# Optimization experiments

Hardware: AMD Instinct MI355X
Metric: run time of the kernel (lower is better)

## Reference

```python
import jax, jax.numpy as jnp
import numpy as np

D = 1024   # hidden
H = 4      # heads
HD = D // H
E = 8      # experts
FF = 4096  # expert ffn dim
CAP_FACTOR = 1.0


def _ln(x, g, b, eps=1e-5):
    mu = jnp.mean(x, -1, keepdims=True)
    v = jnp.mean((x - mu) ** 2, -1, keepdims=True)
    return (x - mu) * jax.lax.rsqrt(v + eps) * g + b


def setup_inputs() -> dict:
    key = jax.random.key(0)
    ks = jax.random.split(key, 8)
    L, N = 1024, 16
    s = 0.02
    return {
        "x": jax.random.normal(ks[0], (L, N, D), jnp.float32),
        "in_proj_w": jax.random.normal(ks[1], (3 * D, D), jnp.float32) * s,
        "in_proj_b": jnp.zeros((3 * D,), jnp.float32),
        "out_proj_w": jax.random.normal(ks[2], (D, D), jnp.float32) * s,
        "out_proj_b": jnp.zeros((D,), jnp.float32),
        "ln1_g": jnp.ones((D,), jnp.float32),
        "ln1_b": jnp.zeros((D,), jnp.float32),
        "ln2_g": jnp.ones((D,), jnp.float32),
        "ln2_b": jnp.zeros((D,), jnp.float32),
        "wg": jax.random.normal(ks[3], (D, E), jnp.float32) * s,
        "w1": jax.random.normal(ks[4], (E, D, FF), jnp.float32) * s,
        "b1": jnp.zeros((E, FF), jnp.float32),
        "w2": jax.random.normal(ks[5], (E, FF, D), jnp.float32) * s,
        "b2": jnp.zeros((E, D), jnp.float32),
    }


def _mha(x, w, b, ow, ob):
    # x: [L, N, D] (torch MultiheadAttention layout, batch_first=False)
    L, N, _ = x.shape
    qkv = x @ w.T + b
    q, k, v = jnp.split(qkv, 3, axis=-1)
    rh = lambda t: t.reshape(L, N, H, HD).transpose(1, 2, 0, 3)  # -> [N,H,L,HD]
    q, k, v = rh(q), rh(k), rh(v)
    scores = jnp.einsum('nhld,nhmd->nhlm', q, k) / np.float32(np.sqrt(HD))
    attn = jax.nn.softmax(scores, axis=-1)
    o = jnp.einsum('nhlm,nhmd->nhld', attn, v).transpose(2, 0, 1, 3).reshape(L, N, D)
    return o @ ow.T + ob


def _moe(x, wg, w1, b1, w2, b2):
    # top-1 switch gating with capacity drop, dispatch, grouped GEMM, combine
    L, N, _ = x.shape
    S = L * N
    cap = int(CAP_FACTOR * S) // E  # 2048
    xf = x.reshape(S, D)
    gates = jax.nn.softmax(xf @ wg, axis=-1)           # [S,E]
    idx = jnp.argmax(gates, axis=-1)                    # [S] top-1 expert
    mask1 = jax.nn.one_hot(idx, E, dtype=x.dtype)       # [S,E]
    # position of each token within its expert's queue
    loc = jnp.sum((jnp.cumsum(mask1, 0) - 1.0) * mask1, -1).astype(jnp.int32)
    keep = loc < cap                                    # capacity drop mask
    gate_val = jnp.take_along_axis(gates, idx[:, None], -1)[:, 0]
    slot = jnp.where(keep, idx.astype(jnp.int32) * cap + loc, E * cap)  # OOB if dropped
    disp = jnp.zeros((E * cap, D), x.dtype).at[slot].set(xf, mode='drop')
    disp = disp.reshape(E, cap, D)
    # expert = Linear(D,FF) -> Linear(FF,D), NO activation between (per source)
    h = jnp.einsum('ecd,edf->ecf', disp, w1) + b1[:, None, :]
    y = (jnp.einsum('ecf,efd->ecd', h, w2) + b2[:, None, :]).reshape(E * cap, D)
    out = jnp.where(keep[:, None], gate_val[:, None] * y[jnp.minimum(slot, E * cap - 1)], 0.0)
    return out.reshape(L, N, D)


def reference(x, in_proj_w, in_proj_b, out_proj_w, out_proj_b,
              ln1_g, ln1_b, ln2_g, ln2_b, wg, w1, b1, w2, b2):
    y1 = _ln(x + _mha(x, in_proj_w, in_proj_b, out_proj_w, out_proj_b), ln1_g, ln1_b)
    y2 = _ln(y1 + _moe(y1, wg, w1, b1, w2, b2), ln2_g, ln2_b)
    return y2
```

## Files before the change

kernel.cpp:

```cpp
#include <hip/hip_runtime.h>
#include <hip/hip_bf16.h>

typedef __bf16 bf16_t;
typedef bf16_t bf16x4 __attribute__((ext_vector_type(4)));
typedef bf16_t bf16x8 __attribute__((ext_vector_type(8)));
typedef float  f32x4  __attribute__((ext_vector_type(4)));
typedef _Float16 half4 __attribute__((ext_vector_type(4)));
typedef _Float16 half8 __attribute__((ext_vector_type(8)));

#define L_  1024
#define N_  16
#define S_  16384
#define D_  1024
#define H_  4
#define HD_ 256
#define E_  8
#define FF_ 4096
#define CAP_ 2048
#define ESLOTS_ (E_*CAP_)
#define TAU_ 0.03f

__device__ __forceinline__ void gload16(const void* g, void* l) {
  __builtin_amdgcn_global_load_lds(
      (const __attribute__((address_space(1))) void*)g,
      (__attribute__((address_space(3))) void*)l,
      16, 0, 0);
}

#define SRC_SWZ(lane) (((lane) & 3) ^ (((lane) >> 3) & 3))

__global__ __launch_bounds__(256) void split2(
    const float* __restrict__ in, _Float16* __restrict__ oh,
    _Float16* __restrict__ ol, long n4)
{
  long i = (long)blockIdx.x * blockDim.x + threadIdx.x;
  long stride = (long)gridDim.x * blockDim.x;
  for (; i < n4; i += stride) {
    float4 v = ((const float4*)in)[i];
    half4 h, l;
    h.x = (_Float16)v.x; l.x = (_Float16)((v.x - (float)h.x) * 4096.0f);
    h.y = (_Float16)v.y; l.y = (_Float16)((v.y - (float)h.y) * 4096.0f);
    h.z = (_Float16)v.z; l.z = (_Float16)((v.z - (float)h.z) * 4096.0f);
    h.w = (_Float16)v.w; l.w = (_Float16)((v.w - (float)h.w) * 4096.0f);
    ((half4*)oh)[i] = h;
    ((half4*)ol)[i] = l;
  }
}

template<int EPI, bool HAS_BIAS, int PROD>
__global__ __launch_bounds__(256) void hgemm3s(
    const _Float16* __restrict__ Ah, const _Float16* __restrict__ Al,
    const _Float16* __restrict__ Bh, const _Float16* __restrict__ Bl,
    float* __restrict__ Cf, _Float16* __restrict__ Ch, _Float16* __restrict__ Cl,
    const float* __restrict__ bias,
    int K, long lda, long ldb, long ldcf, long ldch,
    int Z2, long sA1, long sA2, long sB1, long sB2, long sC1, long sC2, long sBias)
{
  constexpr int NL = (PROD == 3) ? 2 : 1;
  __shared__ _Float16 tA[NL][2][128 * 32];
  __shared__ _Float16 tB[NL][2][64 * 32];
  const int z  = blockIdx.z;
  const int z1 = z / Z2, z2 = z - z1 * Z2;
  const long aoff = (long)z1 * sA1 + (long)z2 * sA2;
  const long boff = (long)z1 * sB1 + (long)z2 * sB2;
  const long coff = (long)z1 * sC1 + (long)z2 * sC2;
  const int brow = blockIdx.y * 128, bcol = blockIdx.x * 64;
  const int tid = threadIdx.x, lane = tid & 63, wid = tid >> 6;
  const int wr = (wid >> 1) * 64, wc = (wid & 1) * 32;
  const int fr = lane & 15;
  const int fqs = (((lane >> 4) ^ ((fr >> 1) & 3)) * 8);

  const bool isA = (wid < 2);
  int limb, dstoff, nch;
  const _Float16* ssrc;
  if constexpr (PROD == 3) {
    limb = wid & 1; nch = isA ? 8 : 4; dstoff = 0;
    ssrc = (wid == 0) ? Ah : (wid == 1) ? Al : (wid == 2) ? Bh : Bl;
  } else {
    limb = 0; nch = isA ? 4 : 2; dstoff = (wid & 1) * nch;
    ssrc = isA ? Ah : Bh;
  }
  const long sld = isA ? lda : ldb;
  const long soff = isA ? aoff : boff;
  int srow = (isA ? brow : bcol) + (lane >> 2);
  if constexpr (PROD == 1) srow += (wid & 1) * (isA ? 64 : 32);
  const _Float16* sbase = ssrc + soff + (long)srow * sld + SRC_SWZ(lane) * 8;

  f32x4 acc0[4][2], acc1[4][2];
#pragma unroll
  for (int mi = 0; mi < 4; ++mi)
#pragma unroll
    for (int ni = 0; ni < 2; ++ni) {
      acc0[mi][ni] = f32x4{0.f, 0.f, 0.f, 0.f};
      acc1[mi][ni] = f32x4{0.f, 0.f, 0.f, 0.f};
    }

  {
    _Float16* d0 = (isA ? &tA[limb][0][0] : &tB[limb][0][0]) + dstoff * 512;
    for (int i = 0; i < nch; ++i)
      gload16(sbase + (long)(16 * i) * sld, d0 + i * 512);
  }
  __syncthreads();

  const int NT = K >> 5;
  for (int t = 0; t < NT; ++t) {
    const int cur = t & 1;
    if (t + 1 < NT) {
      const int k1 = (t + 1) * 32;
      _Float16* d0 = (isA ? &tA[limb][cur ^ 1][0] : &tB[limb][cur ^ 1][0]) + dstoff * 512;
      for (int i = 0; i < nch; ++i)
        gload16(sbase + (long)(16 * i) * sld + k1, d0 + i * 512);
    }

    half8 bh_[2], bl_[2];
#pragma unroll
    for (int ni = 0; ni < 2; ++ni) {
      bh_[ni] = *(const half8*)&tB[0][cur][(wc + ni * 16 + fr) * 32 + fqs];
      if constexpr (PROD == 3)
        bl_[ni] = *(const half8*)&tB[1][cur][(wc + ni * 16 + fr) * 32 + fqs];
    }
    half8 ah_[4], al_[4];
#pragma unroll
    for (int mi = 0; mi < 4; ++mi) {
      ah_[mi] = *(const half8*)&tA[0][cur][(wr + mi * 16 + fr) * 32 + fqs];
      if constexpr (PROD == 3)
        al_[mi] = *(const half8*)&tA[1][cur][(wr + mi * 16 + fr) * 32 + fqs];
    }
#pragma unroll
    for (int mi = 0; mi < 4; ++mi)
#pragma unroll
      for (int ni = 0; ni < 2; ++ni)
        acc0[mi][ni] = __builtin_amdgcn_mfma_f32_16x16x32_f16(ah_[mi], bh_[ni], acc0[mi][ni], 0, 0, 0);
    if constexpr (PROD == 3) {
#pragma unroll
      for (int mi = 0; mi < 4; ++mi)
#pragma unroll
        for (int ni = 0; ni < 2; ++ni)
          acc1[mi][ni] = __builtin_amdgcn_mfma_f32_16x16x32_f16(ah_[mi], bl_[ni], acc1[mi][ni], 0, 0, 0);
#pragma unroll
      for (int mi = 0; mi < 4; ++mi)
#pragma unroll
        for (int ni = 0; ni < 2; ++ni)
          acc1[mi][ni] = __builtin_amdgcn_mfma_f32_16x16x32_f16(al_[mi], bh_[ni], acc1[mi][ni], 0, 0, 0);
    }
    __syncthreads();
  }

#pragma unroll
  for (int mi = 0; mi < 4; ++mi) {
#pragma unroll
    for (int ni = 0; ni < 2; ++ni) {
      int gcol = bcol + wc + ni * 16 + fr;
      float bv = 0.0f;
      if constexpr (HAS_BIAS) bv = bias[(long)z1 * sBias + gcol];
#pragma unroll
      for (int v = 0; v < 4; ++v) {
        int grow = brow + wr + mi * 16 + (lane >> 4) * 4 + v;
        float val = acc0[mi][ni][v] + bv;
        if constexpr (PROD == 3) val += acc1[mi][ni][v] * 0.000244140625f;
        if constexpr (EPI == 0) {
          Cf[coff + (long)grow * ldcf + gcol] = val;
        } else if constexpr (EPI == 1) {
          _Float16 hh = (_Float16)val;
          _Float16 ll = (_Float16)((val - (float)hh) * 4096.0f);
          long ci = coff + (long)grow * ldch + gcol;
          Ch[ci] = hh; Cl[ci] = ll;
        } else if constexpr (EPI == 3) {
          Ch[coff + (long)grow * ldch + gcol] = (_Float16)val;
        } else {
          if (bcol < 2048) {
            _Float16 hh = (_Float16)val;
            _Float16 ll = (_Float16)((val - (float)hh) * 4096.0f);
            long ci = (long)grow * ldch + gcol;
            Ch[ci] = hh; Cl[ci] = ll;
          } else {
            Cf[(long)grow * ldcf + (gcol - 2048)] = val;
          }
        }
      }
    }
  }
}

template<bool OUT_BF16, bool HAS_BIAS>
__global__ __launch_bounds__(512) void bgemm256(
    const bf16_t* __restrict__ A, const bf16_t* __restrict__ B,
    void* __restrict__ Cout, const float* __restrict__ bias,
    int K, long lda, long ldb, long ldc,
    long sA1, long sB1, long sC1, long sBias)
{
  __shared__ bf16_t tA[2][256 * 32];
  __shared__ bf16_t tB[2][128 * 32];
  const int z = blockIdx.z;
  const long coff = (long)z * sC1;
  const int brow = blockIdx.y * 256, bcol = blockIdx.x * 128;
  const int tid = threadIdx.x, lane = tid & 63, wid = tid >> 6;
  const int wr = (wid >> 1) * 64, wc = (wid & 1) * 64;
  const int fr = lane & 15;
  const int fqs = (((lane >> 4) ^ ((fr >> 1) & 3)) * 8);

  const bf16_t* Ab = A + (long)z * sA1;
  const bf16_t* Bb = B + (long)z * sB1;

  const bf16_t* csrc[3];
  bf16_t* cd0[3];
  bf16_t* cd1[3];
  long cld[3];
#pragma unroll
  for (int i = 0; i < 3; ++i) {
    int c = wid * 3 + i;
    bool cA = c < 16;
    const bf16_t* s0 = cA ? Ab : Bb;
    long ld = cA ? lda : ldb;
    int r0 = cA ? (brow + 16 * c) : (bcol + 16 * (c - 16));
    csrc[i] = s0 + (long)(r0 + (lane >> 2)) * ld + SRC_SWZ(lane) * 8;
    cld[i] = ld;
    cd0[i] = cA ? &tA[0][c * 512] : &tB[0][(c - 16) * 512];
    cd1[i] = cA ? &tA[1][c * 512] : &tB[1][(c - 16) * 512];
  }

  f32x4 acc[4][4];
#pragma unroll
  for (int mi = 0; mi < 4; ++mi)
#pragma unroll
    for (int ni = 0; ni < 4; ++ni)
      acc[mi][ni] = f32x4{0.0f, 0.0f, 0.0f, 0.0f};

#pragma unroll
  for (int i = 0; i < 3; ++i) gload16(csrc[i], cd0[i]);
  __syncthreads();

  const int NT = K >> 5;
  for (int t = 0; t < NT; ++t) {
    const int cur = t & 1;
    if (t + 1 < NT) {
      const int k1 = (t + 1) * 32;
#pragma unroll
      for (int i = 0; i < 3; ++i)
        gload16(csrc[i] + k1, cur ? cd0[i] : cd1[i]);
    }
    bf16x8 af[4], bfv[4];
#pragma unroll
    for (int i = 0; i < 4; ++i) {
      af[i]  = *(const bf16x8*)&tA[cur][(wr + i * 16 + fr) * 32 + fqs];
      bfv[i] = *(const bf16x8*)&tB[cur][(wc + i * 16 + fr) * 32 + fqs];
    }
#pragma unroll
    for (int mi = 0; mi < 4; ++mi)
#pragma unroll
      for (int ni = 0; ni < 4; ++ni)
        acc[mi][ni] = __builtin_amdgcn_mfma_f32_16x16x32_bf16(af[mi], bfv[ni], acc[mi][ni], 0, 0, 0);
    __syncthreads();
  }

#pragma unroll
  for (int mi = 0; mi < 4; ++mi) {
#pragma unroll
    for (int ni = 0; ni < 4; ++ni) {
      int gcol = bcol + wc + ni * 16 + fr;
      float bv = 0.0f;
      if constexpr (HAS_BIAS) bv = bias[(long)z * sBias + gcol];
#pragma unroll
      for (int v = 0; v < 4; ++v) {
        int grow = brow + wr + mi * 16 + (lane >> 4) * 4 + v;
        float val = acc[mi][ni][v] + bv;
        long ci = coff + (long)grow * ldc + gcol;
        if constexpr (OUT_BF16) ((bf16_t*)Cout)[ci] = (bf16_t)val;
        else                    ((float*)Cout)[ci]  = val;
      }
    }
  }
}

template<typename TOUT>
__global__ __launch_bounds__(256) void transpose_f32(
    const float* __restrict__ src, TOUT* __restrict__ dst,
    long ld_src, long ld_dst, int Z2,
    long ss1, long ss2, long sd1, long sd2)
{
  __shared__ float t[32][33];
  const int z = blockIdx.z, z1 = z / Z2, z2 = z - z1 * Z2;
  src += (long)z1 * ss1 + (long)z2 * ss2;
  dst += (long)z1 * sd1 + (long)z2 * sd2;
  const int c0 = blockIdx.x * 32, r0 = blockIdx.y * 32;
  const int tx = threadIdx.x & 31, ty = threadIdx.x >> 5;
#pragma unroll
  for (int i = 0; i < 4; ++i)
    t[ty + i * 8][tx] = src[(long)(r0 + ty + i * 8) * ld_src + c0 + tx];
  __syncthreads();
#pragma unroll
  for (int i = 0; i < 4; ++i)
    dst[(long)(c0 + ty + i * 8) * ld_dst + r0 + tx] = (TOUT)t[tx][ty + i * 8];
}

__global__ __launch_bounds__(256) void transpose_split(
    const float* __restrict__ src, _Float16* __restrict__ dh, _Float16* __restrict__ dl,
    long ld_src, long ld_dst, int Z2,
    long ss1, long ss2, long sd1, long sd2)
{
  __shared__ float t[32][33];
  const int z = blockIdx.z, z1 = z / Z2, z2 = z - z1 * Z2;
  src += (long)z1 * ss1 + (long)z2 * ss2;
  dh  += (long)z1 * sd1 + (long)z2 * sd2;
  dl  += (long)z1 * sd1 + (long)z2 * sd2;
  const int c0 = blockIdx.x * 32, r0 = blockIdx.y * 32;
  const int tx = threadIdx.x & 31, ty = threadIdx.x >> 5;
#pragma unroll
  for (int i = 0; i < 4; ++i)
    t[ty + i * 8][tx] = src[(long)(r0 + ty + i * 8) * ld_src + c0 + tx];
  __syncthreads();
#pragma unroll
  for (int i = 0; i < 4; ++i) {
    float v = t[tx][ty + i * 8];
    _Float16 h = (_Float16)v;
    _Float16 l = (_Float16)((v - (float)h) * 4096.0f);
    long idx = (long)(c0 + ty + i * 8) * ld_dst + r0 + tx;
    dh[idx] = h;
    dl[idx] = l;
  }
}

__global__ __launch_bounds__(256) void softmax16(
    _Float16* __restrict__ Sm, float scale)
{
  __shared__ float red[4];
  const long row = blockIdx.x;
  half4* p = (half4*)(Sm + row * 1024);
  const int tid = threadIdx.x;
  half4 hv = p[tid];
  float v0 = (float)hv.x, v1 = (float)hv.y, v2 = (float)hv.z, v3 = (float)hv.w;
  float m = fmaxf(fmaxf(v0, v1), fmaxf(v2, v3));
#pragma unroll
  for (int o = 32; o; o >>= 1) m = fmaxf(m, __shfl_xor(m, o, 64));
  if ((tid & 63) == 0) red[tid >> 6] = m;
  __syncthreads();
  m = fmaxf(fmaxf(red[0], red[1]), fmaxf(red[2], red[3]));
  __syncthreads();
  float e0 = __expf((v0 - m) * scale);
  float e1 = __expf((v1 - m) * scale);
  float e2 = __expf((v2 - m) * scale);
  float e3 = __expf((v3 - m) * scale);
  float s = e0 + e1 + e2 + e3;
#pragma unroll
  for (int o = 32; o; o >>= 1) s += __shfl_xor(s, o, 64);
  if ((tid & 63) == 0) red[tid >> 6] = s;
  __syncthreads();
  s = red[0] + red[1] + red[2] + red[3];
  float inv = 1.0f / s;
  half4 w;
  w.x = (_Float16)(e0 * inv); w.y = (_Float16)(e1 * inv);
  w.z = (_Float16)(e2 * inv); w.w = (_Float16)(e3 * inv);
  p[tid] = w;
}

template<bool WRITE_LO>
__global__ __launch_bounds__(256) void softmax_pack(
    float* __restrict__ Sm, float scale)
{
  __shared__ float red[4];
  const long row = blockIdx.x;
  const float4* p = (const float4*)(Sm + row * 1024);
  const int tid = threadIdx.x;
  float4 v = p[tid];
  float m = fmaxf(fmaxf(v.x, v.y), fmaxf(v.z, v.w));
#pragma unroll
  for (int o = 32; o; o >>= 1) m = fmaxf(m, __shfl_xor(m, o, 64));
  if ((tid & 63) == 0) red[tid >> 6] = m;
  __syncthreads();
  m = fmaxf(fmaxf(red[0], red[1]), fmaxf(red[2], red[3]));
  __syncthreads();
  float e0 = __expf((v.x - m) * scale);
  float e1 = __expf((v.y - m) * scale);
  float e2 = __expf((v.z - m) * scale);
  float e3 = __expf((v.w - m) * scale);
  float s = e0 + e1 + e2 + e3;
#pragma unroll
  for (int o = 32; o; o >>= 1) s += __shfl_xor(s, o, 64);
  if ((tid & 63) == 0) red[tid >> 6] = s;
  __syncthreads();
  s = red[0] + red[1] + red[2] + red[3];
  float inv = 1.0f / s;
  float p0 = e0 * inv, p1 = e1 * inv, p2 = e2 * inv, p3 = e3 * inv;
  half4 h;
  h.x = (_Float16)p0; h.y = (_Float16)p1; h.z = (_Float16)p2; h.w = (_Float16)p3;
  _Float16* base = (_Float16*)Sm + row * 2048;
  ((half4*)base)[tid] = h;
  if constexpr (WRITE_LO) {
    half4 l;
    l.x = (_Float16)((p0 - (float)h.x) * 4096.0f);
    l.y = (_Float16)((p1 - (float)h.y) * 4096.0f);
    l.z = (_Float16)((p2 - (float)h.z) * 4096.0f);
    l.w = (_Float16)((p3 - (float)h.w) * 4096.0f);
    ((half4*)(base + 1024))[tid] = l;
  }
}

__global__ __launch_bounds__(256) void add_ln_gate(
    const float* __restrict__ x, const float* __restrict__ attn,
    const float* __restrict__ g, const float* __restrict__ be,
    const float* __restrict__ wg, bf16_t* __restrict__ yb,
    int* __restrict__ idx, float* __restrict__ gval,
    int* __restrict__ bcnt16, int* __restrict__ blist16)
{
  __shared__ float red[4];
  __shared__ float lred[4][8];
  const long s = blockIdx.x;
  const int tid = threadIdx.x;
  const int lane = tid & 63, w = tid >> 6;
  float4 va = ((const float4*)(x + s * 1024))[tid];
  float4 vb = ((const float4*)(attn + s * 1024))[tid];
  float v0 = va.x + vb.x, v1 = va.y + vb.y, v2 = va.z + vb.z, v3 = va.w + vb.w;
  float sum = v0 + v1 + v2 + v3;
#pragma unroll
  for (int o = 32; o; o >>= 1) sum += __shfl_xor(sum, o, 64);
  if (lane == 0) red[w] = sum;
  __syncthreads();
  float mu = (red[0] + red[1] + red[2] + red[3]) * (1.0f / 1024.0f);
  __syncthreads();
  float d0 = v0 - mu, d1 = v1 - mu, d2 = v2 - mu, d3 = v3 - mu;
  float ss = d0 * d0 + d1 * d1 + d2 * d2 + d3 * d3;
#pragma unroll
  for (int o = 32; o; o >>= 1) ss += __shfl_xor(ss, o, 64);
  if (lane == 0) red[w] = ss;
  __syncthreads();
  float var = (red[0] + red[1] + red[2] + red[3]) * (1.0f / 1024.0f);
  float rstd = rsqrtf(var + 1e-5f);
  float4 vg  = ((const float4*)g)[tid];
  float4 vbe = ((const float4*)be)[tid];
  float y0 = d0 * rstd * vg.x + vbe.x;
  float y1v = d1 * rstd * vg.y + vbe.y;
  float y2v = d2 * rstd * vg.z + vbe.z;
  float y3 = d3 * rstd * vg.w + vbe.w;
  bf16x4 ov = { (bf16_t)y0, (bf16_t)y1v, (bf16_t)y2v, (bf16_t)y3 };
  *(bf16x4*)(yb + s * 1024 + tid * 4) = ov;
  float lg[8];
  const float* w0 = wg + (long)(tid * 4) * 8;
#pragma unroll
  for (int e = 0; e < 8; ++e)
    lg[e] = y0 * w0[e] + y1v * w0[8 + e] + y2v * w0[16 + e] + y3 * w0[24 + e];
#pragma unroll
  for (int e = 0; e < 8; ++e) {
#pragma unroll
    for (int o = 32; o; o >>= 1) lg[e] += __shfl_xor(lg[e], o, 64);
  }
  if (lane == 0) {
#pragma unroll
    for (int e = 0; e < 8; ++e) lred[w][e] = lg[e];
  }
  __syncthreads();
  if (tid == 0) {
    float Lg[8];
#pragma unroll
    for (int e = 0; e < 8; ++e)
      Lg[e] = lred[0][e] + lred[1][e] + lred[2][e] + lred[3][e];
    float best = Lg[0], second = -1e30f; int bi = 0;
#pragma unroll
    for (int e = 1; e < 8; ++e) {
      if (Lg[e] > best) { second = best; best = Lg[e]; bi = e; }
      else if (Lg[e] > second) second = Lg[e];
    }
    float sm = 0.0f;
#pragma unroll
    for (int e = 0; e < 8; ++e) sm += __expf(Lg[e] - best);
    idx[s] = bi;
    gval[s] = 1.0f / sm;
    if (best - second < TAU_) {
      int n = (int)(s & 15);
      int p = atomicAdd(&bcnt16[n], 1);
      if (p < 128) blist16[n * 128 + p] = (int)s;
    }
  }
}

__global__ void zero16(int* __restrict__ p)
{
  if (threadIdx.x < 16) p[threadIdx.x] = 0;
}

__global__ __launch_bounds__(64) void qp_gather(
    const int* __restrict__ bcnt16, const int* __restrict__ blist16,
    const _Float16* __restrict__ QKh, const _Float16* __restrict__ QKl,
    _Float16* __restrict__ Qph, _Float16* __restrict__ Qpl)
{
  const int b = blockIdx.x;
  const int n = b >> 7, p = b & 127;
  const int t = threadIdx.x;
  half8* dh = (half8*)(Qph + (long)b * 1024);
  half8* dl = (half8*)(Qpl + (long)b * 1024);
  int cnt = bcnt16[n]; if (cnt > 128) cnt = 128;
  if (p < cnt) {
    long srow = (long)blist16[b] * 2048;
    const half8* sh = (const half8*)(QKh + srow);
    const half8* sl = (const half8*)(QKl + srow);
    dh[t * 2]     = sh[t * 2];
    dh[t * 2 + 1] = sh[t * 2 + 1];
    dl[t * 2]     = sl[t * 2];
    dl[t * 2 + 1] = sl[t * 2 + 1];
  } else {
    half8 z;
#pragma unroll
    for (int i = 0; i < 8; ++i) z[i] = (_Float16)0.0f;
    dh[t * 2] = z; dh[t * 2 + 1] = z;
    dl[t * 2] = z; dl[t * 2 + 1] = z;
  }
}

__global__ __launch_bounds__(256) void gate_fix(
    const int* __restrict__ bcnt16, const int* __restrict__ blist16,
    const float* __restrict__ attn_p, const float* __restrict__ x,
    const float* __restrict__ g, const float* __restrict__ be,
    const float* __restrict__ wg,
    int* __restrict__ idx, float* __restrict__ gval)
{
  const int b = blockIdx.x;
  const int n = b >> 7, p = b & 127;
  int cnt = bcnt16[n]; if (cnt > 128) cnt = 128;
  if (p >= cnt) return;
  const long s = blist16[b];
  __shared__ float red[4];
  __shared__ float lred[4][8];
  const int tid = threadIdx.x;
  const int lane = tid & 63, w = tid >> 6;
  float4 va = ((const float4*)(x + s * 1024))[tid];
  float4 vb = ((const float4*)(attn_p + (long)b * 1024))[tid];
  float v0 = va.x + vb.x, v1 = va.y + vb.y, v2 = va.z + vb.z, v3 = va.w + vb.w;
  float sum = v0 + v1 + v2 + v3;
#pragma unroll
  for (int o = 32; o; o >>= 1) sum += __shfl_xor(sum, o, 64);
  if (lane == 0) red[w] = sum;
  __syncthreads();
  float mu = (red[0] + red[1] + red[2] + red[3]) * (1.0f / 1024.0f);
  __syncthreads();
  float d0 = v0 - mu, d1 = v1 - mu, d2 = v2 - mu, d3 = v3 - mu;
  float ss = d0 * d0 + d1 * d1 + d2 * d2 + d3 * d3;
#pragma unroll
  for (int o = 32; o; o >>= 1) ss += __shfl_xor(ss, o, 64);
  if (lane == 0) red[w] = ss;
  __syncthreads();
  float var = (red[0] + red[1] + red[2] + red[3]) * (1.0f / 1024.0f);
  float rstd = rsqrtf(var + 1e-5f);
  float4 vg  = ((const float4*)g)[tid];
  float4 vbe = ((const float4*)be)[tid];
  float y0 = d0 * rstd * vg.x + vbe.x;
  float y1v = d1 * rstd * vg.y + vbe.y;
  float y2v = d2 * rstd * vg.z + vbe.z;
  float y3 = d3 * rstd * vg.w + vbe.w;
  float lg[8];
  const float* w0 = wg + (long)(tid * 4) * 8;
#pragma unroll
  for (int e = 0; e < 8; ++e)
    lg[e] = y0 * w0[e] + y1v * w0[8 + e] + y2v * w0[16 + e] + y3 * w0[24 + e];
#pragma unroll
  for (int e = 0; e < 8; ++e) {
#pragma unroll
    for (int o = 32; o; o >>= 1) lg[e] += __shfl_xor(lg[e], o, 64);
  }
  if (lane == 0) {
#pragma unroll
    for (int e = 0; e < 8; ++e) lred[w][e] = lg[e];
  }
  __syncthreads();
  if (tid == 0) {
    float Lg[8];
#pragma unroll
    for (int e = 0; e < 8; ++e)
      Lg[e] = lred[0][e] + lred[1][e] + lred[2][e] + lred[3][e];
    float best = Lg[0]; int bi = 0;
#pragma unroll
    for (int e = 1; e < 8; ++e) { if (Lg[e] > best) { best = Lg[e]; bi = e; } }
    float sm = 0.0f;
#pragma unroll
    for (int e = 0; e < 8; ++e) sm += __expf(Lg[e] - best);
    idx[s] = bi;
    gval[s] = 1.0f / sm;
  }
}

__global__ __launch_bounds__(256) void combine_ln(
    const bf16_t* __restrict__ y1b, const bf16_t* __restrict__ ymoe,
    const int* __restrict__ slot, const float* __restrict__ gval,
    const float* __restrict__ g, const float* __restrict__ be,
    float* __restrict__ out)
{
  __shared__ float red[4];
  const long s = blockIdx.x;
  const int tid = threadIdx.x;
  const int lane = tid & 63, w = tid >> 6;
  int sl = slot[s];
  bool keep = sl < ESLOTS_;
  float gv = keep ? gval[s] : 0.0f;
  long mrow = keep ? (long)sl * 1024 : 0;
  bf16x4 ya = *(const bf16x4*)(y1b + s * 1024 + tid * 4);
  bf16x4 ym = *(const bf16x4*)(ymoe + mrow + tid * 4);
  float v0 = (float)ya[0] + gv * (float)ym[0];
  float v1 = (float)ya[1] + gv * (float)ym[1];
  float v2 = (float)ya[2] + gv * (float)ym[2];
  float v3 = (float)ya[3] + gv * (float)ym[3];
  float sum = v0 + v1 + v2 + v3;
#pragma unroll
  for (int o = 32; o; o >>= 1) sum += __shfl_xor(sum, o, 64);
  if (lane == 0) red[w] = sum;
  __syncthreads();
  float mu = (red[0] + red[1] + red[2] + red[3]) * (1.0f / 1024.0f);
  __syncthreads();
  float d0 = v0 - mu, d1 = v1 - mu, d2 = v2 - mu, d3 = v3 - mu;
  float ss = d0 * d0 + d1 * d1 + d2 * d2 + d3 * d3;
#pragma unroll
  for (int o = 32; o; o >>= 1) ss += __shfl_xor(ss, o, 64);
  if (lane == 0) red[w] = ss;
  __syncthreads();
  float var = (red[0] + red[1] + red[2] + red[3]) * (1.0f / 1024.0f);
  float rstd = rsqrtf(var + 1e-5f);
  float4 vg  = ((const float4*)g)[tid];
  float4 vbe = ((const float4*)be)[tid];
  float4 ov = {d0 * rstd * vg.x + vbe.x, d1 * rstd * vg.y + vbe.y,
               d2 * rstd * vg.z + vbe.z, d3 * rstd * vg.w + vbe.w};
  ((float4*)(out + s * 1024))[tid] = ov;
}

__global__ __launch_bounds__(1024) void route_scan(
    const int* __restrict__ idx, int* __restrict__ slot, int* __restrict__ tfs)
{
  __shared__ int c_lds[8][1024];
  const int tid = threadIdx.x;
  const int lane = tid & 63, wid = tid >> 6;

  for (int j = tid; j < ESLOTS_; j += 1024) tfs[j] = -1;

  int myc[8] = {0, 0, 0, 0, 0, 0, 0, 0};
  for (int j = 0; j < 16; ++j) {
    int e = idx[tid * 16 + j];
    myc[e]++;
  }
#pragma unroll
  for (int e = 0; e < 8; ++e) c_lds[e][tid] = myc[e];
  __syncthreads();

  if (wid < 8) {
    int carry = 0;
    for (int cb = 0; cb < 1024; cb += 64) {
      int v = c_lds[wid][cb + lane];
#pragma unroll
      for (int o = 1; o < 64; o <<= 1) {
        int t = __shfl_up(v, o, 64);
        if (lane >= o) v += t;
      }
      v += carry;
      c_lds[wid][cb + lane] = v;
      carry = __shfl(v, 63, 64);
    }
  }
  __syncthreads();

  int run[8] = {0, 0, 0, 0, 0, 0, 0, 0};
  for (int j = 0; j < 16; ++j) {
    int s = tid * 16 + j;
    int e = idx[s];
    int excl = c_lds[e][tid] - myc[e];
    int loc = excl + run[e];
    run[e]++;
    int sl = (loc < CAP_) ? e * CAP_ + loc : ESLOTS_;
    slot[s] = sl;
    if (sl < ESLOTS_) tfs[sl] = s;
  }
}

__global__ void dispatch_rows(
    const int* __restrict__ tfs, const bf16_t* __restrict__ y1b,
    bf16_t* __restrict__ disp)
{
  const int row = blockIdx.x;
  const int t = tfs[row];
  bf16x8* d = (bf16x8*)(disp + (long)row * 1024);
  if (t >= 0) {
    const bf16x8* sp = (const bf16x8*)(y1b + (long)t * 1024);
    d[threadIdx.x] = sp[threadIdx.x];
  } else {
    bf16x8 zv;
#pragma unroll
    for (int i = 0; i < 8; ++i) zv[i] = (bf16_t)0.0f;
    d[threadIdx.x] = zv;
  }
}

__global__ void fill_val(float* __restrict__ p, float v, long n)
{
  long i = (long)blockIdx.x * blockDim.x + threadIdx.x;
  long stride = (long)gridDim.x * blockDim.x;
  for (; i < n; i += stride) p[i] = v;
}

extern "C" void kernel_launch(void* const* d_in, const int* in_sizes, int n_in,
                              void* d_out, int out_size, void* d_ws, size_t ws_size,
                              hipStream_t stream)
{
  const float* x    = (const float*)d_in[0];
  const float* Wqkv = (const float*)d_in[1];
  const float* bqkv = (const float*)d_in[2];
  const float* Wo   = (const float*)d_in[3];
  const float* bo   = (const float*)d_in[4];
  const float* g1   = (const float*)d_in[5];
  const float* b1n  = (const float*)d_in[6];
  const float* g2   = (const float*)d_in[7];
  const float* b2n  = (const float*)d_in[8];
  const float* wg   = (const float*)d_in[9];
  const float* w1   = (const float*)d_in[10];
  const float* b1e  = (const float*)d_in[11];
  const float* w2   = (const float*)d_in[12];
  const float* b2e  = (const float*)d_in[13];
  float* out = (float*)d_out;

  const size_t MB = 1ull << 20;
  const size_t REQUIRED = 384 * MB;
  if (ws_size < REQUIRED) {
    fill_val<<<2048, 256, 0, stream>>>(out, (float)(ws_size >> 20), (long)out_size);
    return;
  }

  char* ws = (char*)d_ws;
  _Float16* Xh   = (_Float16*)(ws + 0);
  _Float16* Xl   = (_Float16*)(ws + 32 * MB);
  _Float16* Wqh  = (_Float16*)(ws + 64 * MB);
  _Float16* Wql  = (_Float16*)(ws + 70 * MB);
  _Float16* scores16 = (_Float16*)(ws + 0);
  _Float16* Woh  = (_Float16*)(ws + 64 * MB);
  _Float16* Wol  = (_Float16*)(ws + 66 * MB);
  _Float16* QKh  = (_Float16*)(ws + 80 * MB);
  _Float16* QKl  = (_Float16*)(ws + 144 * MB);
  float*    Vf32 = (float*)(ws + 208 * MB);
  _Float16* oh   = (_Float16*)(ws + 208 * MB);
  _Float16* vTh  = (_Float16*)(ws + 272 * MB);
  _Float16* vTl  = (_Float16*)(ws + 304 * MB);
  float*    attn = (float*)(ws + 0);
  bf16_t*   y1b  = (bf16_t*)(ws + 208 * MB);
  float*    scp   = (float*)(ws + 0);
  _Float16* Qph   = (_Float16*)(ws + 32 * MB);
  _Float16* Qpl   = (_Float16*)(ws + 36 * MB);
  _Float16* o_ph  = (_Float16*)(ws + 40 * MB);
  _Float16* o_pl  = (_Float16*)(ws + 44 * MB);
  float*    attnp = (float*)(ws + 48 * MB);
  int*      idx  = (int*)(ws + 336 * MB);
  int*      slot = idx + S_;
  float*    gval = (float*)(slot + S_);
  int*      tfs  = (int*)(gval + S_);
  int*      bcnt16  = tfs + S_;
  int*      blist16 = bcnt16 + 16;
  bf16_t*   disp = (bf16_t*)(ws + 272 * MB);
  bf16_t*   W1t  = (bf16_t*)(ws + 0);
  bf16_t*   W2t  = (bf16_t*)(ws + 0);
  bf16_t*   h    = (bf16_t*)(ws + 80 * MB);
  bf16_t*   ymoe = (bf16_t*)(ws + 304 * MB);

  zero16<<<1, 64, 0, stream>>>(bcnt16);

  split2<<<4096, 256, 0, stream>>>(x, Xh, Xl, (long)S_ * D_ / 4);
  split2<<<2048, 256, 0, stream>>>(Wqkv, Wqh, Wql, (long)3 * D_ * D_ / 4);

  hgemm3s<2, true, 3><<<dim3(48, 128, 1), 256, 0, stream>>>(
      Xh, Xl, Wqh, Wql, Vf32, QKh, QKl, bqkv,
      D_, D_, D_, D_, 2 * D_,
      1, 0, 0, 0, 0, 0, 0, 0);

  split2<<<1024, 256, 0, stream>>>(Wo, Woh, Wol, (long)D_ * D_ / 4);

  transpose_split<<<dim3(HD_ / 32, L_ / 32, 64), 256, 0, stream>>>(
      Vf32, vTh, vTl, (long)N_ * D_, L_,
      H_, D_, HD_, (long)H_ * HD_ * L_, (long)HD_ * L_);

  for (int g = 0; g < 2; ++g) {
    const long qko = (long)g * 8 * 2048;
    hgemm3s<3, false, 1><<<dim3(16, 8, 32), 256, 0, stream>>>(
        QKh + qko, QKl + qko, QKh + qko + 1024, QKl + qko + 1024,
        nullptr, scores16, nullptr, nullptr,
        HD_, (long)N_ * 2048, (long)N_ * 2048, 0, L_,
        H_, 2048, 256, 2048, 256, (long)H_ * L_ * L_, (long)L_ * L_, 0);
    softmax16<<<8 * H_ * L_, 256, 0, stream>>>(scores16, 0.0625f);
    hgemm3s<3, false, 1><<<dim3(4, 8, 32), 256, 0, stream>>>(
        scores16, nullptr,
        vTh + (long)g * 8 * H_ * HD_ * L_, vTl + (long)g * 8 * H_ * HD_ * L_,
        nullptr, oh + (long)g * 8 * D_, nullptr, nullptr,
        L_, L_, L_, 0, (long)N_ * D_,
        H_, (long)H_ * L_ * L_, (long)L_ * L_,
        (long)H_ * HD_ * L_, (long)HD_ * L_, D_, HD_, 0);
  }

  hgemm3s<0, true, 1><<<dim3(16, 128, 1), 256, 0, stream>>>(
      oh, nullptr, Woh, Wol, attn, nullptr, nullptr, bo,
      D_, D_, D_, D_, 0,
      1, 0, 0, 0, 0, 0, 0, 0);

  add_ln_gate<<<S_, 256, 0, stream>>>(x, attn, g1, b1n, wg, y1b,
                                      idx, gval, bcnt16, blist16);

  qp_gather<<<2048, 64, 0, stream>>>(bcnt16, blist16, QKh, QKl, Qph, Qpl);
  hgemm3s<0, false, 3><<<dim3(16, 1, 64), 256, 0, stream>>>(
      Qph, Qpl, QKh + 1024, QKl + 1024, scp, nullptr, nullptr, nullptr,
      HD_, 1024, (long)N_ * 2048, 1024, 0,
      4, (long)128 * 1024, 256, 2048, 256,
      (long)4 * 128 * 1024, (long)128 * 1024, 0);
  softmax_pack<true><<<64 * 128, 256, 0, stream>>>(scp, 0.0625f);
  hgemm3s<1, false, 3><<<dim3(4, 1, 64), 256, 0, stream>>>(
      (_Float16*)scp, (_Float16*)scp + 1024, vTh, vTl,
      nullptr, o_ph, o_pl, nullptr,
      L_, 2048, L_, 0, 1024,
      4, (long)4 * 128 * 2048, (long)128 * 2048,
      (long)H_ * HD_ * L_, (long)HD_ * L_,
      (long)128 * 1024, 256, 0);
  hgemm3s<0, true, 3><<<dim3(16, 16, 1), 256, 0, stream>>>(
      o_ph, o_pl, Woh, Wol, attnp, nullptr, nullptr, bo,
      D_, D_, D_, D_, 0,
      1, 0, 0, 0, 0, 0, 0, 0);
  gate_fix<<<2048, 256, 0, stream>>>(bcnt16, blist16, attnp, x,
                                     g1, b1n, wg, idx, gval);

  route_scan<<<1, 1024, 0, stream>>>(idx, slot, tfs);

  dispatch_rows<<<ESLOTS_, 128, 0, stream>>>(tfs, y1b, disp);

  transpose_f32<bf16_t><<<dim3(FF_ / 32, D_ / 32, E_), 256, 0, stream>>>(
      w1, W1t, FF_, D_, 1, (long)D_ * FF_, 0, (long)FF_ * D_, 0);

  bgemm256<true, true><<<dim3(32, 8, 8), 512, 0, stream>>>(
      disp, W1t, h, b1e, D_, D_, D_, FF_,
      (long)CAP_ * D_, (long)FF_ * D_, (long)CAP_ * FF_, FF_);

  transpose_f32<bf16_t><<<dim3(D_ / 32, FF_ / 32, E_), 256, 0, stream>>>(
      w2, W2t, D_, FF_, 1, (long)FF_ * D_, 0, (long)D_ * FF_, 0);

  bgemm256<true, true><<<dim3(8, 8, 8), 512, 0, stream>>>(
      h, W2t, ymoe, b2e, FF_, FF_, FF_, D_,
      (long)CAP_ * FF_, (long)D_ * FF_, (long)CAP_ * D_, D_);

  combine_ln<<<S_, 256, 0, stream>>>(y1b, ymoe, slot, gval, g2, b2n, out);
}
```

Measured before the change: 1.588 ms.

## Triple-buffer LDS tiles with prefetch depth two in single-limb and expert GEMMs

Switches the single-product fp16 GEMM path and the expert bf16 GEMM to a three-stage LDS ring. Tiles are prefetched two k-steps ahead, and the full __syncthreads is replaced by a partial vmcnt wait plus s_barrier, so global loads overlap compute more deeply. The expert GEMM also moves from 256x128 tiles with 512 threads to 128x128 tiles with 256 threads, doubling the grid. The cost is more LDS per block and hand-tuned vmcnt counts that must match the number of issued loads.

Result: faster. 1.499 ms (-5.6%).

```diff
diff --git a/kernel.cpp b/kernel.cpp
--- a/kernel.cpp
+++ b/kernel.cpp
@@ -56,9 +56,10 @@
     int K, long lda, long ldb, long ldcf, long ldch,
     int Z2, long sA1, long sA2, long sB1, long sB2, long sC1, long sC2, long sBias)
 {
-  constexpr int NL = (PROD == 3) ? 2 : 1;
-  __shared__ _Float16 tA[NL][2][128 * 32];
-  __shared__ _Float16 tB[NL][2][64 * 32];
+  constexpr int NL   = (PROD == 3) ? 2 : 1;
+  constexpr int NBUF = (PROD == 3) ? 2 : 3;
+  __shared__ _Float16 tA[NL][NBUF][128 * 32];
+  __shared__ _Float16 tB[NL][NBUF][64 * 32];
   const int z  = blockIdx.z;
   const int z1 = z / Z2, z2 = z - z1 * Z2;
   const long aoff = (long)z1 * sA1 + (long)z2 * sA2;
@@ -95,43 +96,42 @@
       acc1[mi][ni] = f32x4{0.f, 0.f, 0.f, 0.f};
     }
 
-  {
-    _Float16* d0 = (isA ? &tA[limb][0][0] : &tB[limb][0][0]) + dstoff * 512;
-    for (int i = 0; i < nch; ++i)
-      gload16(sbase + (long)(16 * i) * sld, d0 + i * 512);
-  }
-  __syncthreads();
-
   const int NT = K >> 5;
-  for (int t = 0; t < NT; ++t) {
-    const int cur = t & 1;
-    if (t + 1 < NT) {
-      const int k1 = (t + 1) * 32;
-      _Float16* d0 = (isA ? &tA[limb][cur ^ 1][0] : &tB[limb][cur ^ 1][0]) + dstoff * 512;
+
+  if constexpr (PROD == 3) {
+    {
+      _Float16* d0 = (isA ? &tA[limb][0][0] : &tB[limb][0][0]) + dstoff * 512;
       for (int i = 0; i < nch; ++i)
-        gload16(sbase + (long)(16 * i) * sld + k1, d0 + i * 512);
-    }
-
-    half8 bh_[2], bl_[2];
-#pragma unroll
-    for (int ni = 0; ni < 2; ++ni) {
-      bh_[ni] = *(const half8*)&tB[0][cur][(wc + ni * 16 + fr) * 32 + fqs];
-      if constexpr (PROD == 3)
+        gload16(sbase + (long)(16 * i) * sld, d0 + i * 512);
+    }
+    __syncthreads();
+
+    for (int t = 0; t < NT; ++t) {
+      const int cur = t & 1;
+      if (t + 1 < NT) {
+        const int k1 = (t + 1) * 32;
+        _Float16* d0 = (isA ? &tA[limb][cur ^ 1][0] : &tB[limb][cur ^ 1][0]) + dstoff * 512;
+        for (int i = 0; i < nch; ++i)
+          gload16(sbase + (long)(16 * i) * sld + k1, d0 + i * 512);
+      }
+
+      half8 bh_[2], bl_[2];
+#pragma unroll
+      for (int ni = 0; ni < 2; ++ni) {
+        bh_[ni] = *(const half8*)&tB[0][cur][(wc + ni * 16 + fr) * 32 + fqs];
         bl_[ni] = *(const half8*)&tB[1][cur][(wc + ni * 16 + fr) * 32 + fqs];
-    }
-    half8 ah_[4], al_[4];
-#pragma unroll
-    for (int mi = 0; mi < 4; ++mi) {
-      ah_[mi] = *(const half8*)&tA[0][cur][(wr + mi * 16 + fr) * 32 + fqs];
-      if constexpr (PROD == 3)
+      }
+      half8 ah_[4], al_[4];
+#pragma unroll
+      for (int mi = 0; mi < 4; ++mi) {
+        ah_[mi] = *(const half8*)&tA[0][cur][(wr + mi * 16 + fr) * 32 + fqs];
         al_[mi] = *(const half8*)&tA[1][cur][(wr + mi * 16 + fr) * 32 + fqs];
-    }
-#pragma unroll
-    for (int mi = 0; mi < 4; ++mi)
-#pragma unroll
-      for (int ni = 0; ni < 2; ++ni)
-        acc0[mi][ni] = __builtin_amdgcn_mfma_f32_16x16x32_f16(ah_[mi], bh_[ni], acc0[mi][ni], 0, 0, 0);
-    if constexpr (PROD == 3) {
+      }
+#pragma unroll
+      for (int mi = 0; mi < 4; ++mi)
+#pragma unroll
+        for (int ni = 0; ni < 2; ++ni)
+          acc0[mi][ni] = __builtin_amdgcn_mfma_f32_16x16x32_f16(ah_[mi], bh_[ni], acc0[mi][ni], 0, 0, 0);
 #pragma unroll
       for (int mi = 0; mi < 4; ++mi)
 #pragma unroll
@@ -142,8 +142,55 @@
 #pragma unroll
         for (int ni = 0; ni < 2; ++ni)
           acc1[mi][ni] = __builtin_amdgcn_mfma_f32_16x16x32_f16(al_[mi], bh_[ni], acc1[mi][ni], 0, 0, 0);
-    }
-    __syncthreads();
+      __syncthreads();
+    }
+  } else {
+    {
+      _Float16* d0 = (isA ? &tA[0][0][0] : &tB[0][0][0]) + dstoff * 512;
+      for (int i = 0; i < nch; ++i)
+        gload16(sbase + (long)(16 * i) * sld, d0 + i * 512);
+      _Float16* d1 = (isA ? &tA[0][1][0] : &tB[0][1][0]) + dstoff * 512;
+      for (int i = 0; i < nch; ++i)
+        gload16(sbase + (long)(16 * i) * sld + 32, d1 + i * 512);
+    }
+    if (isA) asm volatile("s_waitcnt vmcnt(4)" ::: "memory");
+    else     asm volatile("s_waitcnt vmcnt(2)" ::: "memory");
+    __builtin_amdgcn_s_barrier();
+
+    for (int t = 0; t < NT; ++t) {
+      const int b = t % 3;
+      if (t + 2 < NT) {
+        const int k2 = (t + 2) * 32;
+        const int b2 = (t + 2) % 3;
+        _Float16* d0 = (isA ? &tA[0][b2][0] : &tB[0][b2][0]) + dstoff * 512;
+        for (int i = 0; i < nch; ++i)
+          gload16(sbase + (long)(16 * i) * sld + k2, d0 + i * 512);
+      }
+
+      half8 bh_[2];
+#pragma unroll
+      for (int ni = 0; ni < 2; ++ni)
+        bh_[ni] = *(const half8*)&tB[0][b][(wc + ni * 16 + fr) * 32 + fqs];
+      half8 ah_[4];
+#pragma unroll
+      for (int mi = 0; mi < 4; ++mi)
+        ah_[mi] = *(const half8*)&tA[0][b][(wr + mi * 16 + fr) * 32 + fqs];
+#pragma unroll
+      for (int mi = 0; mi < 4; ++mi)
+#pragma unroll
+        for (int ni = 0; ni < 2; ++ni)
+          acc0[mi][ni] = __builtin_amdgcn_mfma_f32_16x16x32_f16(ah_[mi], bh_[ni], acc0[mi][ni], 0, 0, 0);
+
+      if (t + 1 < NT) {
+        if (t + 2 < NT) {
+          if (isA) asm volatile("s_waitcnt vmcnt(4)" ::: "memory");
+          else     asm volatile("s_waitcnt vmcnt(2)" ::: "memory");
+        } else {
+          asm volatile("s_waitcnt vmcnt(0)" ::: "memory");
+        }
+        __builtin_amdgcn_s_barrier();
+      }
+    }
   }
 
 #pragma unroll
@@ -183,41 +230,26 @@
 }
 
 template<bool OUT_BF16, bool HAS_BIAS>
-__global__ __launch_bounds__(512) void bgemm256(
+__global__ __launch_bounds__(256) void bgemm16(
     const bf16_t* __restrict__ A, const bf16_t* __restrict__ B,
     void* __restrict__ Cout, const float* __restrict__ bias,
     int K, long lda, long ldb, long ldc,
     long sA1, long sB1, long sC1, long sBias)
 {
-  __shared__ bf16_t tA[2][256 * 32];
-  __shared__ bf16_t tB[2][128 * 32];
+  __shared__ bf16_t tiles[2][3][128 * 32];
   const int z = blockIdx.z;
   const long coff = (long)z * sC1;
-  const int brow = blockIdx.y * 256, bcol = blockIdx.x * 128;
+  const int brow = blockIdx.y * 128, bcol = blockIdx.x * 128;
   const int tid = threadIdx.x, lane = tid & 63, wid = tid >> 6;
   const int wr = (wid >> 1) * 64, wc = (wid & 1) * 64;
   const int fr = lane & 15;
   const int fqs = (((lane >> 4) ^ ((fr >> 1) & 3)) * 8);
 
-  const bf16_t* Ab = A + (long)z * sA1;
-  const bf16_t* Bb = B + (long)z * sB1;
-
-  const bf16_t* csrc[3];
-  bf16_t* cd0[3];
-  bf16_t* cd1[3];
-  long cld[3];
-#pragma unroll
-  for (int i = 0; i < 3; ++i) {
-    int c = wid * 3 + i;
-    bool cA = c < 16;
-    const bf16_t* s0 = cA ? Ab : Bb;
-    long ld = cA ? lda : ldb;
-    int r0 = cA ? (brow + 16 * c) : (bcol + 16 * (c - 16));
-    csrc[i] = s0 + (long)(r0 + (lane >> 2)) * ld + SRC_SWZ(lane) * 8;
-    cld[i] = ld;
-    cd0[i] = cA ? &tA[0][c * 512] : &tB[0][(c - 16) * 512];
-    cd1[i] = cA ? &tA[1][c * 512] : &tB[1][(c - 16) * 512];
-  }
+  const bf16_t* src0 = (wid < 2) ? (A + (long)z * sA1) : (B + (long)z * sB1);
+  const long ld = (wid < 2) ? lda : ldb;
+  const int  rb = ((wid < 2) ? brow : bcol) + 64 * (wid & 1) + (lane >> 2);
+  const bf16_t* srcbase = src0 + (long)rb * ld + SRC_SWZ(lane) * 8;
+  const int tsel = wid >> 1, halfsel = wid & 1;
 
   f32x4 acc[4][4];
 #pragma unroll
@@ -226,31 +258,44 @@
     for (int ni = 0; ni < 4; ++ni)
       acc[mi][ni] = f32x4{0.0f, 0.0f, 0.0f, 0.0f};
 
-#pragma unroll
-  for (int i = 0; i < 3; ++i) gload16(csrc[i], cd0[i]);
-  __syncthreads();
-
   const int NT = K >> 5;
+
+#pragma unroll
+  for (int i = 0; i < 4; ++i)
+    gload16(srcbase + (long)(16 * i) * ld, &tiles[tsel][0][(4 * halfsel + i) * 512]);
+#pragma unroll
+  for (int i = 0; i < 4; ++i)
+    gload16(srcbase + (long)(16 * i) * ld + 32, &tiles[tsel][1][(4 * halfsel + i) * 512]);
+  asm volatile("s_waitcnt vmcnt(4)" ::: "memory");
+  __builtin_amdgcn_s_barrier();
+
   for (int t = 0; t < NT; ++t) {
-    const int cur = t & 1;
-    if (t + 1 < NT) {
-      const int k1 = (t + 1) * 32;
-#pragma unroll
-      for (int i = 0; i < 3; ++i)
-        gload16(csrc[i] + k1, cur ? cd0[i] : cd1[i]);
-    }
+    const int b = t % 3;
+    if (t + 2 < NT) {
+      const int k2 = (t + 2) * 32;
+      const int b2 = (t + 2) % 3;
+#pragma unroll
+      for (int i = 0; i < 4; ++i)
+        gload16(srcbase + (long)(16 * i) * ld + k2, &tiles[tsel][b2][(4 * halfsel + i) * 512]);
+    }
+
     bf16x8 af[4], bfv[4];
 #pragma unroll
     for (int i = 0; i < 4; ++i) {
-      af[i]  = *(const bf16x8*)&tA[cur][(wr + i * 16 + fr) * 32 + fqs];
-      bfv[i] = *(const bf16x8*)&tB[cur][(wc + i * 16 + fr) * 32 + fqs];
+      af[i]  = *(const bf16x8*)&tiles[0][b][(wr + i * 16 + fr) * 32 + fqs];
+      bfv[i] = *(const bf16x8*)&tiles[1][b][(wc + i * 16 + fr) * 32 + fqs];
     }
 #pragma unroll
     for (int mi = 0; mi < 4; ++mi)
 #pragma unroll
       for (int ni = 0; ni < 4; ++ni)
         acc[mi][ni] = __builtin_amdgcn_mfma_f32_16x16x32_bf16(af[mi], bfv[ni], acc[mi][ni], 0, 0, 0);
-    __syncthreads();
+
+    if (t + 1 < NT) {
+      if (t + 2 < NT) asm volatile("s_waitcnt vmcnt(4)" ::: "memory");
+      else            asm volatile("s_waitcnt vmcnt(0)" ::: "memory");
+      __builtin_amdgcn_s_barrier();
+    }
   }
 
 #pragma unroll
@@ -820,14 +865,14 @@
   transpose_f32<bf16_t><<<dim3(FF_ / 32, D_ / 32, E_), 256, 0, stream>>>(
       w1, W1t, FF_, D_, 1, (long)D_ * FF_, 0, (long)FF_ * D_, 0);
 
-  bgemm256<true, true><<<dim3(32, 8, 8), 512, 0, stream>>>(
+  bgemm16<true, true><<<dim3(32, 16, 8), 256, 0, stream>>>(
       disp, W1t, h, b1e, D_, D_, D_, FF_,
       (long)CAP_ * D_, (long)FF_ * D_, (long)CAP_ * FF_, FF_);
 
   transpose_f32<bf16_t><<<dim3(D_ / 32, FF_ / 32, E_), 256, 0, stream>>>(
       w2, W2t, D_, FF_, 1, (long)FF_ * D_, 0, (long)D_ * FF_, 0);
 
-  bgemm256<true, true><<<dim3(8, 8, 8), 512, 0, stream>>>(
+  bgemm16<true, true><<<dim3(8, 16, 8), 256, 0, stream>>>(
       h, W2t, ymoe, b2e, FF_, FF_, FF_, D_,
       (long)CAP_ * FF_, (long)D_ * FF_, (long)CAP_ * D_, D_);
 
```
